# Optimization experiments

Hardware: AMD Instinct MI355X
Metric: run time of the kernel (lower is better)

The kernel has to match this reference:

```python
import jax, jax.numpy as jnp
import numpy as np

W, H = 1920, 1080
WEIGHT = 0.2          # self.weight
CONT_W = 0.1          # continuity_weight
RANK_M = 1e-4         # ranking_margin
CONT_M = 1e-4         # continuity_margin
SAMPLE_RATIO = 0.25
R = 3                 # knn_crop_radius
PAD_VAL = -1000000.0


def setup_inputs() -> dict:
    key = jax.random.key(0)
    k1, k2, k3 = jax.random.split(key, 3)
    return {
        "target_depths": jax.random.uniform(k1, (1, H * W), dtype=jnp.float32) * 100.0,
        "render_depths": jax.random.uniform(k2, (H * W,), dtype=jnp.float32) * 100.0,
        "valid_mask": jax.random.randint(k3, (1, H * W, 1), 0, 2, dtype=jnp.int32),
        "width": W,
        "height": H,
    }


def _sample_depth_loss_indices(depths, width, height, valid_mask, n_samples,
                               rank_patch_size, r, key):
    win = 2 * r + 1                      # 7
    top_n = int(0.3 * win * win + 1)     # 15
    ks = jax.random.split(key, 5)
    sy = jax.random.randint(ks[0], (n_samples, 1), 0, height - rank_patch_size)
    sx = jax.random.randint(ks[1], (n_samples, 1), 0, width - rank_patch_size)
    sy = sy + jax.random.randint(ks[2], (n_samples, 2), 0, rank_patch_size)
    sx = sx + jax.random.randint(ks[3], (n_samples, 2), 0, rank_patch_size)
    sample_idx = sy * width + sx                               # (n, 2)
    sampled_depth = depths[0][sample_idx]                      # (n, 2)

    padded = jnp.pad(depths.reshape(height, width), r, constant_values=PAD_VAL)
    dy = jnp.repeat(jnp.arange(win), win)                      # (49,) row offsets
    dx = jnp.tile(jnp.arange(win), win)                        # (49,) col offsets
    # padded coords: (y - r + dy) + r == y + dy
    py = sy[..., None] + dy                                    # (n, 2, 49)
    px = sx[..., None] + dx
    depth_crops = padded[py, px]                               # (n, 2, 49)

    sorted_crop_idx = jnp.argsort(jnp.abs(depth_crops - sampled_depth[..., None]), axis=-1)
    nbr_sample = jax.random.randint(ks[4], (n_samples, 2, 1), 1, top_n)
    rel = jnp.take_along_axis(sorted_crop_idx, nbr_sample, axis=-1)[..., 0]  # (n, 2)
    ny = sy - r + rel // win
    nx = sx - r + rel % win
    neighbours_idx = ny * width + nx                           # (n, 2)

    vm = valid_mask[0].astype(bool)                            # (H*W, C)
    samples_mask = vm[sample_idx].any(-1).all(-1)              # (n,)
    neighbours_mask = vm[neighbours_idx].any(-1).all(-1)
    full_mask = samples_mask & neighbours_mask

    # per-pair descending sort by sampled target depth
    order = jnp.argsort(-sampled_depth, axis=-1)
    s_sorted = jnp.take_along_axis(sample_idx, order, axis=-1)
    n_sorted = jnp.take_along_axis(neighbours_idx, order, axis=-1)
    idx4 = jnp.concatenate([s_sorted, n_sorted], axis=-1)      # (n, 4)
    return idx4, full_mask


def reference(target_depths, render_depths, valid_mask, width, height):
    n_samples = int(width * height * SAMPLE_RATIO)
    rank_patch_size = width // 8
    idx4, mask = _sample_depth_loss_indices(
        target_depths, width, height, valid_mask, n_samples, rank_patch_size,
        R, jax.random.key(42))
    d = render_depths[idx4].reshape(-1, 2, 2)                  # (n, 2, 2)
    rank = jnp.maximum(d[:, 0, 0] - d[:, 0, 1] + RANK_M, 0.0)  # (n,)
    cont = jnp.maximum(jnp.abs(d[:, 0, :] - d[:, 1, :]) - CONT_M, 0.0)  # (n, 2)
    # masked means == torch's boolean filtering followed by .mean()
    m = mask.astype(rank.dtype)
    denom = jnp.maximum(m.sum(), 1.0)
    rank_mean = (rank * m).sum() / denom
    cont_mean = (cont * m[:, None]).sum() / (denom * 2.0)
    return jnp.stack([WEIGHT * rank_mean, WEIGHT * CONT_W * cont_mean])
```

## Files before the change

### kernel.cpp

```cpp
#include <hip/hip_runtime.h>
#include <stdint.h>


#define IMG_W 1920
#define IMG_H 1080
#define N_PIX (IMG_W * IMG_H)
#define N_SAMP 518400
#define SEG    2025
#define PAD_VAL (-1000000.0f)
#define PW 968
#define PH 1088
#define PAD16 0xC974u

typedef uint32_t u32x4 __attribute__((ext_vector_type(4)));

struct Keys { uint32_t k[5][2][2]; };

static __host__ __device__ inline void tf2x32(uint32_t k0, uint32_t k1,
                                              uint32_t x0, uint32_t x1,
                                              uint32_t& o0, uint32_t& o1)
{
  const uint32_t ks2 = k0 ^ k1 ^ 0x1BD11BDAu;
  x0 += k0; x1 += k1;
#define TFR(r) { x0 += x1; x1 = (x1 << (r)) | (x1 >> (32 - (r))); x1 ^= x0; }
  TFR(13) TFR(15) TFR(26) TFR(6)
  x0 += k1;  x1 += ks2 + 1u;
  TFR(17) TFR(29) TFR(16) TFR(24)
  x0 += ks2; x1 += k0 + 2u;
  TFR(13) TFR(15) TFR(26) TFR(6)
  x0 += k0;  x1 += k1 + 3u;
  TFR(17) TFR(29) TFR(16) TFR(24)
  x0 += k1;  x1 += ks2 + 4u;
  TFR(13) TFR(15) TFR(26) TFR(6)
  x0 += ks2; x1 += k0 + 5u;
#undef TFR
  o0 = x0; o1 = x1;
}

__device__ __forceinline__ uint32_t jrbits(const uint32_t kk[2], uint32_t f)
{
  uint32_t a, b;
  tf2x32(kk[0], kk[1], 0u, f, a, b);
  return a ^ b;
}

__device__ __forceinline__ uint32_t jrandint(const Keys& K, int r, uint32_t f,
                                             uint32_t span)
{
  const uint32_t hi = jrbits(K.k[r][0], f);
  const uint32_t lo = jrbits(K.k[r][1], f);
  uint32_t m = 65536u % span;
  m = (m * m) % span;
  return ((hi % span) * m + (lo % span)) % span;
}

static void compute_keys(Keys& K)
{
  uint32_t ks[5][2];
  for (uint32_t t = 0; t < 5; t++) {
    uint32_t a, b; tf2x32(0u, 42u, 0u, t, a, b);
    ks[t][0] = a; ks[t][1] = b;
  }
  for (int r = 0; r < 5; r++) {
    uint32_t a, b;
    tf2x32(ks[r][0], ks[r][1], 0u, 0u, a, b); K.k[r][0][0] = a; K.k[r][0][1] = b;
    tf2x32(ks[r][0], ks[r][1], 0u, 1u, a, b); K.k[r][1][0] = a; K.k[r][1][1] = b;
  }
}

__device__ __forceinline__ bool bittest(const unsigned long long* __restrict__ vb,
                                        uint32_t idx)
{
  return ((vb[idx >> 6] >> (idx & 63u)) & 1ull) != 0ull;
}

__global__ __launch_bounds__(256) void gs_bitpack(
    const int* __restrict__ vmask,
    unsigned long long* __restrict__ vbits)
{
  const uint32_t gid = blockIdx.x * 256u + threadIdx.x;
  const unsigned long long ball = __ballot(vmask[gid] != 0);
  if ((threadIdx.x & 63u) == 0) vbits[gid >> 6] = ball;
}

__global__ __launch_bounds__(256) void gs_pack16(
    const float* __restrict__ tgt,
    uint32_t* __restrict__ t16p)
{
  const uint32_t w = blockIdx.x * 256u + threadIdx.x;
  if (w >= (uint32_t)(PW * PH)) return;
  const uint32_t wy = w / PW, wx = w % PW;
  const int sy  = (int)wy - 4;
  const int sx0 = 2 * (int)wx - 4;
  uint32_t lo = PAD16, hi = PAD16;
  if (sy >= 0 && sy < IMG_H) {
    const uint32_t* src = (const uint32_t*)tgt + (size_t)sy * IMG_W;
    if (sx0     >= 0 && sx0     < IMG_W) lo = src[sx0] >> 16;
    if (sx0 + 1 >= 0 && sx0 + 1 < IMG_W) hi = src[sx0 + 1] >> 16;
  }
  t16p[w] = lo | (hi << 16);
}

__global__ __launch_bounds__(256) void gs_sample(
    const unsigned long long* __restrict__ vbits,
    uint32_t* __restrict__ bcount,
    unsigned long long* __restrict__ wlist,
    Keys K)
{
  __shared__ unsigned long long ent[256];
  __shared__ uint32_t scnt[4];

  const uint32_t tid  = threadIdx.x;
  const uint32_t lane = tid & 63u;
  const uint32_t wave = tid >> 6;
  const uint32_t ui   = blockIdx.x * 256u + tid;

  const uint32_t syb  = jrandint(K, 0, ui, 840u);
  const uint32_t sxb  = jrandint(K, 1, ui, 1680u);
  const uint32_t oy0  = jrandint(K, 2, 2u * ui,      240u);
  const uint32_t oy1  = jrandint(K, 2, 2u * ui + 1u, 240u);
  const uint32_t ox0  = jrandint(K, 3, 2u * ui,      240u);
  const uint32_t ox1  = jrandint(K, 3, 2u * ui + 1u, 240u);
  const uint32_t nb0  = jrandint(K, 4, 2u * ui,      14u);
  const uint32_t nb1  = jrandint(K, 4, 2u * ui + 1u, 14u);
  asm volatile("" :: "v"(syb), "v"(sxb), "v"(oy0), "v"(oy1),
                     "v"(ox0), "v"(ox1), "v"(nb0), "v"(nb1));

  const uint32_t sy0 = syb + oy0, sy1 = syb + oy1;
  const uint32_t sx0 = sxb + ox0, sx1 = sxb + ox1;
  const bool ok = bittest(vbits, sy0 * IMG_W + sx0) &&
                  bittest(vbits, sy1 * IMG_W + sx1);

  const unsigned long long ball = __ballot(ok);
  if (lane == 0) scnt[wave] = (uint32_t)__popcll(ball);
  __syncthreads();

  uint32_t base = 0;
#pragma unroll
  for (uint32_t w = 0; w < 4; w++) if (w < wave) base += scnt[w];
  const uint32_t nsurv = scnt[0] + scnt[1] + scnt[2] + scnt[3];

  if (ok) {
    const uint32_t pos = base + (uint32_t)__popcll(ball & ((1ull << lane) - 1ull));
    ent[pos] = ((unsigned long long)(1u + nb1) << 48) |
               ((unsigned long long)(1u + nb0) << 44) |
               ((unsigned long long)sy0 << 33) | ((unsigned long long)sx0 << 22) |
               ((unsigned long long)sy1 << 11) |  (unsigned long long)sx1;
  }
  if (tid == 0) bcount[blockIdx.x] = nsurv;
  __syncthreads();

  unsigned long long* wb = wlist + (size_t)blockIdx.x * 256u;
  for (uint32_t t = tid; t < nsurv; t += 256u)
    wb[t] = ent[t];
}

__device__ __forceinline__ int crop_neighbor16(
    const uint32_t* __restrict__ t16p, int sy, int sx,
    float& sd_out, uint32_t nbr)
{
  const int prow0 = sy + 1;
  const int pcol  = sx + 1;
  const int ex    = pcol & ~1;
  const uint32_t s = (uint32_t)(pcol & 1);
  const uint32_t* p = t16p + (size_t)prow0 * PW + (ex >> 1);

  u32x4 R0, R1, R2, R3, R4, R5, R6;
  asm volatile(
      "global_load_dwordx4 %0, %7, off\n\t"
      "global_load_dwordx4 %1, %8, off\n\t"
      "global_load_dwordx4 %2, %9, off\n\t"
      "global_load_dwordx4 %3, %10, off\n\t"
      "global_load_dwordx4 %4, %11, off\n\t"
      "global_load_dwordx4 %5, %12, off\n\t"
      "global_load_dwordx4 %6, %13, off\n\t"
      "s_waitcnt vmcnt(0)"
      : "=&v"(R0), "=&v"(R1), "=&v"(R2), "=&v"(R3),
        "=&v"(R4), "=&v"(R5), "=&v"(R6)
      : "v"(p), "v"(p + PW), "v"(p + 2 * PW), "v"(p + 3 * PW),
        "v"(p + 4 * PW), "v"(p + 5 * PW), "v"(p + 6 * PW));

  const uint32_t sdbits = s ? (R3[2] << 16) : (R3[1] & 0xFFFF0000u);
  const float sd = __uint_as_float(sdbits);
  sd_out = sd;

  const u32x4 R[7] = { R0, R1, R2, R3, R4, R5, R6 };

  uint32_t arr[15];
#pragma unroll
  for (int t = 0; t < 15; t++) arr[t] = 0xFFFFFFFFu;

#pragma unroll
  for (int r = 0; r < 7; r++) {
    const u32x4 W = R[r];
#pragma unroll
    for (int c = 0; c < 7; c++) {
      uint32_t bits;
      if (c & 1) bits = s ? (W[(c + 1) >> 1] << 16) : (W[c >> 1] & 0xFFFF0000u);
      else       bits = s ? (W[c >> 1] & 0xFFFF0000u) : (W[c >> 1] << 16);
      const float v = __uint_as_float(bits);
      const int q = r * 7 + c;
      uint32_t key = (__float_as_uint(v - sd) & 0x7FFFFFC0u) | (uint32_t)q;
      const int depth = (q + 1 < 15) ? (q + 1) : 15;
#pragma unroll
      for (int t = 0; t < 15; t++) {
        if (t < depth) {
          const uint32_t lo = min(key, arr[t]);
          const uint32_t hi = max(key, arr[t]);
          arr[t] = lo; key = hi;
        }
      }
    }
  }

  uint32_t relkey = 0;
#pragma unroll
  for (int t = 1; t < 15; t++)
    if ((uint32_t)t == nbr) relkey = arr[t];
  const uint32_t rel = relkey & 63u;
  return (sy - 3 + (int)(rel / 7u)) * IMG_W + (sx - 3 + (int)(rel % 7u));
}

__global__ __launch_bounds__(256, 4) void gs_crop(
    const uint32_t* __restrict__ t16p,
    const float* __restrict__ rnd,
    const unsigned long long* __restrict__ vbits,
    const uint32_t* __restrict__ bcount,
    const unsigned long long* __restrict__ wlist,
    float* __restrict__ acc)
{
  __shared__ float partial[12];
  const uint32_t tid  = threadIdx.x;
  const uint32_t lane = tid & 63u;
  const uint32_t wave = tid >> 6;

  const uint32_t seg0 = 2u * blockIdx.x;
  const uint32_t c0 = bcount[seg0];
  const uint32_t c1 = (seg0 + 1 < SEG) ? bcount[seg0 + 1] : 0;
  const uint32_t m  = 2u * (c0 + c1);

  float rank_a = 0.f, cont_a = 0.f, cnt_a = 0.f;
  for (uint32_t t = tid; t < ((m + 255u) & ~255u); t += 256u) {
    float sd = 0.f, r = 0.f, q = 0.f;
    bool v = false;
    if (t < m) {
      const uint32_t tc0 = 2u * c0;
      const unsigned long long e = (t < tc0)
          ? wlist[(size_t)seg0 * 256u + (t >> 1)]
          : wlist[(size_t)(seg0 + 1) * 256u + ((t - tc0) >> 1)];
      const int j = (int)(t & 1u);
      const int sy  = j ? (int)((e >> 11) & 2047u) : (int)((e >> 33) & 2047u);
      const int sx  = j ? (int)( e        & 2047u) : (int)((e >> 22) & 2047u);
      const uint32_t nbr = j ? (uint32_t)((e >> 48) & 15u)
                             : (uint32_t)((e >> 44) & 15u);
      r = rnd[sy * IMG_W + sx];
      const int nidx = crop_neighbor16(t16p, sy, sx, sd, nbr);
      v = bittest(vbits, (uint32_t)nidx);
      q = rnd[nidx];
    }

    const float psd = __shfl_xor(sd, 1);
    const float pr  = __shfl_xor(r, 1);
    const bool  pv  = (bool)__shfl_xor((int)v, 1);
    const bool pairok = (t < m) && v && pv;

    cont_a += pairok ? fmaxf(fabsf(r - q) - 1e-4f, 0.f) : 0.f;
    if (pairok && ((t & 1u) == 0)) {
      const bool keep = sd >= psd;
      const float ra = keep ? r : pr;
      const float rb = keep ? pr : r;
      rank_a += fmaxf(ra - rb + 1e-4f, 0.f);
      cnt_a  += 1.f;
    }
  }

#pragma unroll
  for (int off = 32; off > 0; off >>= 1) {
    rank_a += __shfl_down(rank_a, off);
    cont_a += __shfl_down(cont_a, off);
    cnt_a  += __shfl_down(cnt_a, off);
  }
  if (lane == 0) {
    partial[wave * 3 + 0] = rank_a;
    partial[wave * 3 + 1] = cont_a;
    partial[wave * 3 + 2] = cnt_a;
  }
  __syncthreads();
  if (tid < 3) {
    const float sm = partial[tid] + partial[3 + tid] +
                     partial[6 + tid] + partial[9 + tid];
    atomicAdd(acc + tid, sm);
  }
}

__device__ __forceinline__ int crop_neighbor32(const float* __restrict__ tgt,
                                               int sy, int sx, float sd,
                                               uint32_t nbr)
{
  float v[7][8];
  const bool interior = (sy >= 3) && (sy <= IMG_H - 4) &&
                        (sx >= 3) && (sx <= IMG_W - 5);
  if (interior) {
    const float* p = tgt + (sy - 3) * IMG_W + (sx - 3);
#pragma unroll
    for (int r = 0; r < 7; r++)
      __builtin_memcpy(&v[r][0], p + r * IMG_W, 32);
  } else {
#pragma unroll
    for (int r = 0; r < 7; r++) {
      const int yy = sy - 3 + r;
      const bool rok = (yy >= 0) && (yy < IMG_H);
#pragma unroll
      for (int c = 0; c < 8; c++) {
        const int xx = sx - 3 + c;
        const bool okc = rok && (c < 7) && (xx >= 0) && (xx < IMG_W);
        v[r][c] = okc ? tgt[yy * IMG_W + xx] : PAD_VAL;
      }
    }
  }
  uint32_t arr[15];
#pragma unroll
  for (int t = 0; t < 15; t++) arr[t] = 0xFFFFFFFFu;
#pragma unroll
  for (int r = 0; r < 7; r++) {
#pragma unroll
    for (int c = 0; c < 7; c++) {
      const int q = r * 7 + c;
      uint32_t key = (__float_as_uint(v[r][c] - sd) & 0x7FFFFFC0u) | (uint32_t)q;
      const int depth = (q + 1 < 15) ? (q + 1) : 15;
#pragma unroll
      for (int t = 0; t < 15; t++) {
        if (t < depth) {
          const uint32_t lo = min(key, arr[t]);
          const uint32_t hi = max(key, arr[t]);
          arr[t] = lo; key = hi;
        }
      }
    }
  }
  uint32_t relkey = 0;
#pragma unroll
  for (int t = 1; t < 15; t++)
    if ((uint32_t)t == nbr) relkey = arr[t];
  const uint32_t rel = relkey & 63u;
  return (sy - 3 + (int)(rel / 7u)) * IMG_W + (sx - 3 + (int)(rel % 7u));
}

__global__ __launch_bounds__(256, 2) void gs_fused(
    const float* __restrict__ tgt,
    const float* __restrict__ rnd,
    const int*   __restrict__ vmask,
    float* __restrict__ acc,
    Keys K)
{
  __shared__ float partial[12];
  const uint32_t tid  = threadIdx.x;
  const uint32_t lane = tid & 63u;
  const uint32_t wave = tid >> 6;
  const uint32_t ui   = blockIdx.x * 256u + tid;

  float rank_c = 0.f, cont_c = 0.f, cnt_c = 0.f;
  if (ui < N_SAMP) {
    const uint32_t syb = jrandint(K, 0, ui, 840u);
    const uint32_t sxb = jrandint(K, 1, ui, 1680u);
    int sy[2], sx[2], sidx[2];
    float sd[2];
    bool sm = true;
#pragma unroll
    for (int j = 0; j < 2; j++) {
      sy[j] = (int)(syb + jrandint(K, 2, 2u * ui + (uint32_t)j, 240u));
      sx[j] = (int)(sxb + jrandint(K, 3, 2u * ui + (uint32_t)j, 240u));
      sidx[j] = sy[j] * IMG_W + sx[j];
      sd[j] = tgt[sidx[j]];
      sm = sm && (vmask[sidx[j]] != 0);
    }
    if (sm) {
      int nidx[2]; bool nm = true;
#pragma unroll
      for (int j = 0; j < 2; j++) {
        const uint32_t nbr = 1u + jrandint(K, 4, 2u * ui + (uint32_t)j, 14u);
        nidx[j] = crop_neighbor32(tgt, sy[j], sx[j], sd[j], nbr);
        nm = nm && (vmask[nidx[j]] != 0);
      }
      if (nm) {
        const float r0 = rnd[sidx[0]], r1 = rnd[sidx[1]];
        const float q0 = rnd[nidx[0]], q1 = rnd[nidx[1]];
        const bool keep = sd[0] >= sd[1];
        const float ra = keep ? r0 : r1;
        const float rb = keep ? r1 : r0;
        rank_c = fmaxf(ra - rb + 1e-4f, 0.f);
        cont_c = fmaxf(fabsf(r0 - q0) - 1e-4f, 0.f)
               + fmaxf(fabsf(r1 - q1) - 1e-4f, 0.f);
        cnt_c = 1.f;
      }
    }
  }
#pragma unroll
  for (int off = 32; off > 0; off >>= 1) {
    rank_c += __shfl_down(rank_c, off);
    cont_c += __shfl_down(cont_c, off);
    cnt_c  += __shfl_down(cnt_c, off);
  }
  if (lane == 0) {
    partial[wave * 3 + 0] = rank_c;
    partial[wave * 3 + 1] = cont_c;
    partial[wave * 3 + 2] = cnt_c;
  }
  __syncthreads();
  if (tid < 3) {
    const float sm2 = partial[tid] + partial[3 + tid] +
                      partial[6 + tid] + partial[9 + tid];
    atomicAdd(acc + tid, sm2);
  }
}

__global__ void gs_finalize(const float* __restrict__ acc, float* __restrict__ out)
{
  const float denom = fmaxf(acc[2], 1.0f);
  out[0] = 0.2f * (acc[0] / denom);
  out[1] = 0.2f * 0.1f * (acc[1] / (denom * 2.0f));
}

extern "C" void kernel_launch(void* const* d_in, const int* in_sizes, int n_in,
                              void* d_out, int out_size, void* d_ws, size_t ws_size,
                              hipStream_t stream)
{
  (void)in_sizes; (void)n_in; (void)out_size;
  const float* tgt   = (const float*)d_in[0];
  const float* rnd   = (const float*)d_in[1];
  const int*   vmask = (const int*)d_in[2];
  float* out = (float*)d_out;

  char* p = (char*)d_ws;
  float*    acc   = (float*)p;
  unsigned long long* vbits = (unsigned long long*)(p + 16);
  uint32_t* t16p  = (uint32_t*)(p + 16 + 259200);
  uint32_t* bcount = (uint32_t*)(p + 16 + 259200 + 4213504);
  unsigned long long* wlist =
      (unsigned long long*)(p + 16 + 259200 + 4213504 + 8112);
  const size_t need = 16 + 259200 + 4213504 + 8112 + (size_t)SEG * 256 * 8;

  Keys K;
  compute_keys(K);

  hipMemsetAsync(acc, 0, 16, stream);

  if (ws_size >= need) {
    gs_bitpack<<<N_PIX / 256, 256, 0, stream>>>(vmask, vbits);
    gs_pack16<<<(PW * PH + 255) / 256, 256, 0, stream>>>(tgt, t16p);
    gs_sample<<<SEG, 256, 0, stream>>>(vbits, bcount, wlist, K);
    gs_crop<<<(SEG + 1) / 2, 256, 0, stream>>>(t16p, rnd, vbits, bcount,
                                               wlist, acc);
  } else {
    gs_fused<<<N_SAMP / 256, 256, 0, stream>>>(tgt, rnd, vmask, acc, K);
  }
  gs_finalize<<<1, 1, 0, stream>>>(acc, out);
}
```

Before: 68.57 us.

## Fuse sampling, crop and finalize into one kernel; merge prep kernels

Merges bitpack and pack16 into a single prep kernel that also zeroes the accumulator header, replacing the memset. The sampling and crop stages now run in one kernel that compacts surviving pairs in shared memory, and the last block to finish writes the final outputs, so the global worklist round-trip and three launches go away. The per-neighbour random draw is recomputed after compaction rather than stored, and launch bounds drop to 2 blocks per SM. The cost is more shared memory, lower occupancy and a serialised last-block finalize.

New measurement: 85.64 us. 1.25x slower.

```diff
diff --git a/kernel.cpp b/kernel.cpp
--- a/kernel.cpp
+++ b/kernel.cpp
@@ -6,13 +6,14 @@
 #define IMG_H 1080
 #define N_PIX (IMG_W * IMG_H)
 #define N_SAMP 518400
-#define SEG    2025
+#define MAIN_BLKS 1013
 #define PAD_VAL (-1000000.0f)
 #define PW 968
 #define PH 1088
 #define PAD16 0xC974u
 
 typedef uint32_t u32x4 __attribute__((ext_vector_type(4)));
+typedef unsigned long long ull;
 
 struct Keys { uint32_t k[5][2][2]; };
 
@@ -68,91 +69,35 @@
   }
 }
 
-__device__ __forceinline__ bool bittest(const unsigned long long* __restrict__ vb,
-                                        uint32_t idx)
+__device__ __forceinline__ bool bittest(const ull* __restrict__ vb, uint32_t idx)
 {
   return ((vb[idx >> 6] >> (idx & 63u)) & 1ull) != 0ull;
 }
 
-__global__ __launch_bounds__(256) void gs_bitpack(
-    const int* __restrict__ vmask,
-    unsigned long long* __restrict__ vbits)
+__global__ __launch_bounds__(256) void gs_prep(
+    const int*   __restrict__ vmask,
+    const float* __restrict__ tgt,
+    ull*      __restrict__ vbits,
+    uint32_t* __restrict__ t16p,
+    uint32_t* __restrict__ hdr)
 {
   const uint32_t gid = blockIdx.x * 256u + threadIdx.x;
-  const unsigned long long ball = __ballot(vmask[gid] != 0);
+  const ull ball = __ballot(vmask[gid] != 0);
   if ((threadIdx.x & 63u) == 0) vbits[gid >> 6] = ball;
-}
-
-__global__ __launch_bounds__(256) void gs_pack16(
-    const float* __restrict__ tgt,
-    uint32_t* __restrict__ t16p)
-{
-  const uint32_t w = blockIdx.x * 256u + threadIdx.x;
-  if (w >= (uint32_t)(PW * PH)) return;
-  const uint32_t wy = w / PW, wx = w % PW;
-  const int sy  = (int)wy - 4;
-  const int sx0 = 2 * (int)wx - 4;
-  uint32_t lo = PAD16, hi = PAD16;
-  if (sy >= 0 && sy < IMG_H) {
-    const uint32_t* src = (const uint32_t*)tgt + (size_t)sy * IMG_W;
-    if (sx0     >= 0 && sx0     < IMG_W) lo = src[sx0] >> 16;
-    if (sx0 + 1 >= 0 && sx0 + 1 < IMG_W) hi = src[sx0 + 1] >> 16;
-  }
-  t16p[w] = lo | (hi << 16);
-}
-
-__global__ __launch_bounds__(256) void gs_sample(
-    const unsigned long long* __restrict__ vbits,
-    uint32_t* __restrict__ bcount,
-    unsigned long long* __restrict__ wlist,
-    Keys K)
-{
-  __shared__ unsigned long long ent[256];
-  __shared__ uint32_t scnt[4];
-
-  const uint32_t tid  = threadIdx.x;
-  const uint32_t lane = tid & 63u;
-  const uint32_t wave = tid >> 6;
-  const uint32_t ui   = blockIdx.x * 256u + tid;
-
-  const uint32_t syb  = jrandint(K, 0, ui, 840u);
-  const uint32_t sxb  = jrandint(K, 1, ui, 1680u);
-  const uint32_t oy0  = jrandint(K, 2, 2u * ui,      240u);
-  const uint32_t oy1  = jrandint(K, 2, 2u * ui + 1u, 240u);
-  const uint32_t ox0  = jrandint(K, 3, 2u * ui,      240u);
-  const uint32_t ox1  = jrandint(K, 3, 2u * ui + 1u, 240u);
-  const uint32_t nb0  = jrandint(K, 4, 2u * ui,      14u);
-  const uint32_t nb1  = jrandint(K, 4, 2u * ui + 1u, 14u);
-  asm volatile("" :: "v"(syb), "v"(sxb), "v"(oy0), "v"(oy1),
-                     "v"(ox0), "v"(ox1), "v"(nb0), "v"(nb1));
-
-  const uint32_t sy0 = syb + oy0, sy1 = syb + oy1;
-  const uint32_t sx0 = sxb + ox0, sx1 = sxb + ox1;
-  const bool ok = bittest(vbits, sy0 * IMG_W + sx0) &&
-                  bittest(vbits, sy1 * IMG_W + sx1);
-
-  const unsigned long long ball = __ballot(ok);
-  if (lane == 0) scnt[wave] = (uint32_t)__popcll(ball);
-  __syncthreads();
-
-  uint32_t base = 0;
-#pragma unroll
-  for (uint32_t w = 0; w < 4; w++) if (w < wave) base += scnt[w];
-  const uint32_t nsurv = scnt[0] + scnt[1] + scnt[2] + scnt[3];
-
-  if (ok) {
-    const uint32_t pos = base + (uint32_t)__popcll(ball & ((1ull << lane) - 1ull));
-    ent[pos] = ((unsigned long long)(1u + nb1) << 48) |
-               ((unsigned long long)(1u + nb0) << 44) |
-               ((unsigned long long)sy0 << 33) | ((unsigned long long)sx0 << 22) |
-               ((unsigned long long)sy1 << 11) |  (unsigned long long)sx1;
-  }
-  if (tid == 0) bcount[blockIdx.x] = nsurv;
-  __syncthreads();
-
-  unsigned long long* wb = wlist + (size_t)blockIdx.x * 256u;
-  for (uint32_t t = tid; t < nsurv; t += 256u)
-    wb[t] = ent[t];
+
+  if (gid < (uint32_t)(PW * PH)) {
+    const uint32_t wy = gid / PW, wx = gid % PW;
+    const int sy  = (int)wy - 4;
+    const int sx0 = 2 * (int)wx - 4;
+    uint32_t lo = PAD16, hi = PAD16;
+    if (sy >= 0 && sy < IMG_H) {
+      const uint32_t* src = (const uint32_t*)tgt + (size_t)sy * IMG_W;
+      if (sx0     >= 0 && sx0     < IMG_W) lo = src[sx0] >> 16;
+      if (sx0 + 1 >= 0 && sx0 + 1 < IMG_W) hi = src[sx0 + 1] >> 16;
+    }
+    t16p[gid] = lo | (hi << 16);
+  }
+  if (gid < 4) hdr[gid] = 0;
 }
 
 __device__ __forceinline__ int crop_neighbor16(
@@ -221,75 +166,138 @@
   return (sy - 3 + (int)(rel / 7u)) * IMG_W + (sx - 3 + (int)(rel % 7u));
 }
 
-__global__ __launch_bounds__(256, 4) void gs_crop(
+__global__ __launch_bounds__(256, 2) void gs_main(
     const uint32_t* __restrict__ t16p,
     const float* __restrict__ rnd,
-    const unsigned long long* __restrict__ vbits,
-    const uint32_t* __restrict__ bcount,
-    const unsigned long long* __restrict__ wlist,
-    float* __restrict__ acc)
-{
-  __shared__ float partial[12];
+    const ull*   __restrict__ vbits,
+    float* __restrict__ acc,
+    float* __restrict__ out,
+    Keys K)
+{
+  __shared__ ull      ent[512];
+  __shared__ float    res_sd[1024];
+  __shared__ int      res_ni[1024];
+  __shared__ uint32_t scnt[8];
+  __shared__ float    partial[12];
+
   const uint32_t tid  = threadIdx.x;
   const uint32_t lane = tid & 63u;
   const uint32_t wave = tid >> 6;
 
-  const uint32_t seg0 = 2u * blockIdx.x;
-  const uint32_t c0 = bcount[seg0];
-  const uint32_t c1 = (seg0 + 1 < SEG) ? bcount[seg0 + 1] : 0;
-  const uint32_t m  = 2u * (c0 + c1);
-
-  float rank_a = 0.f, cont_a = 0.f, cnt_a = 0.f;
-  for (uint32_t t = tid; t < ((m + 255u) & ~255u); t += 256u) {
-    float sd = 0.f, r = 0.f, q = 0.f;
-    bool v = false;
-    if (t < m) {
-      const uint32_t tc0 = 2u * c0;
-      const unsigned long long e = (t < tc0)
-          ? wlist[(size_t)seg0 * 256u + (t >> 1)]
-          : wlist[(size_t)(seg0 + 1) * 256u + ((t - tc0) >> 1)];
-      const int j = (int)(t & 1u);
-      const int sy  = j ? (int)((e >> 11) & 2047u) : (int)((e >> 33) & 2047u);
-      const int sx  = j ? (int)( e        & 2047u) : (int)((e >> 22) & 2047u);
-      const uint32_t nbr = j ? (uint32_t)((e >> 48) & 15u)
-                             : (uint32_t)((e >> 44) & 15u);
-      r = rnd[sy * IMG_W + sx];
-      const int nidx = crop_neighbor16(t16p, sy, sx, sd, nbr);
-      v = bittest(vbits, (uint32_t)nidx);
-      q = rnd[nidx];
-    }
-
-    const float psd = __shfl_xor(sd, 1);
-    const float pr  = __shfl_xor(r, 1);
-    const bool  pv  = (bool)__shfl_xor((int)v, 1);
-    const bool pairok = (t < m) && v && pv;
-
-    cont_a += pairok ? fmaxf(fabsf(r - q) - 1e-4f, 0.f) : 0.f;
-    if (pairok && ((t & 1u) == 0)) {
-      const bool keep = sd >= psd;
-      const float ra = keep ? r : pr;
-      const float rb = keep ? pr : r;
-      rank_a += fmaxf(ra - rb + 1e-4f, 0.f);
-      cnt_a  += 1.f;
+  ull eb[2];
+  bool ok[2];
+#pragma unroll
+  for (int h = 0; h < 2; h++) {
+    const uint32_t ui = blockIdx.x * 512u + (uint32_t)h * 256u + tid;
+    bool o = false;
+    ull ee = 0;
+    if (ui < N_SAMP) {
+      const uint32_t syb = jrandint(K, 0, ui, 840u);
+      const uint32_t sxb = jrandint(K, 1, ui, 1680u);
+      const uint32_t oy0 = jrandint(K, 2, 2u * ui,      240u);
+      const uint32_t oy1 = jrandint(K, 2, 2u * ui + 1u, 240u);
+      const uint32_t ox0 = jrandint(K, 3, 2u * ui,      240u);
+      const uint32_t ox1 = jrandint(K, 3, 2u * ui + 1u, 240u);
+      asm volatile("" :: "v"(syb), "v"(sxb), "v"(oy0), "v"(oy1),
+                         "v"(ox0), "v"(ox1));
+      const uint32_t sy0 = syb + oy0, sy1 = syb + oy1;
+      const uint32_t sx0 = sxb + ox0, sx1 = sxb + ox1;
+      o = bittest(vbits, sy0 * IMG_W + sx0) &&
+          bittest(vbits, sy1 * IMG_W + sx1);
+      ee = ((ull)ui << 44) |
+           ((ull)sy0 << 33) | ((ull)sx0 << 22) |
+           ((ull)sy1 << 11) |  (ull)sx1;
+    }
+    ok[h] = o; eb[h] = ee;
+  }
+
+  const ull b0 = __ballot(ok[0]);
+  const ull b1 = __ballot(ok[1]);
+  if (lane == 0) {
+    scnt[wave]     = (uint32_t)__popcll(b0);
+    scnt[4 + wave] = (uint32_t)__popcll(b1);
+  }
+  __syncthreads();
+
+  uint32_t base0 = 0, sum0 = 0, base1 = 0, nsurv = 0;
+#pragma unroll
+  for (uint32_t w = 0; w < 4; w++) {
+    if (w < wave) { base0 += scnt[w]; base1 += scnt[4 + w]; }
+    sum0  += scnt[w];
+    nsurv += scnt[w] + scnt[4 + w];
+  }
+  base1 += sum0;
+
+  if (ok[0]) ent[base0 + (uint32_t)__popcll(b0 & ((1ull << lane) - 1ull))] = eb[0];
+  if (ok[1]) ent[base1 + (uint32_t)__popcll(b1 & ((1ull << lane) - 1ull))] = eb[1];
+  __syncthreads();
+
+  for (uint32_t t = tid; t < 2u * nsurv; t += 256u) {
+    const ull ee = ent[t >> 1];
+    const int jj = (int)(t & 1u);
+    const uint32_t eui = (uint32_t)(ee >> 44);
+    const int sy = jj ? (int)((ee >> 11) & 2047u) : (int)((ee >> 33) & 2047u);
+    const int sx = jj ? (int)( ee        & 2047u) : (int)((ee >> 22) & 2047u);
+    const uint32_t nbr = 1u + jrandint(K, 4, 2u * eui + (uint32_t)jj, 14u);
+    float sd;
+    const int nidx = crop_neighbor16(t16p, sy, sx, sd, nbr);
+    res_sd[t] = sd;
+    res_ni[t] = bittest(vbits, (uint32_t)nidx) ? nidx : -1;
+  }
+  __syncthreads();
+
+  float rank_c = 0.f, cont_c = 0.f, cnt_c = 0.f;
+  for (uint32_t sI = tid; sI < nsurv; sI += 256u) {
+    const int n0 = res_ni[2u * sI], n1 = res_ni[2u * sI + 1u];
+    if ((n0 >= 0) && (n1 >= 0)) {
+      const ull ee = ent[sI];
+      const int esy0 = (int)((ee >> 33) & 2047u), esx0 = (int)((ee >> 22) & 2047u);
+      const int esy1 = (int)((ee >> 11) & 2047u), esx1 = (int)( ee        & 2047u);
+      const float r0 = rnd[esy0 * IMG_W + esx0];
+      const float r1 = rnd[esy1 * IMG_W + esx1];
+      const float q0 = rnd[n0], q1 = rnd[n1];
+      const float sd0 = res_sd[2u * sI], sd1 = res_sd[2u * sI + 1u];
+      const bool keep = sd0 >= sd1;
+      const float ra = keep ? r0 : r1;
+      const float rb = keep ? r1 : r0;
+      rank_c += fmaxf(ra - rb + 1e-4f, 0.f);
+      cont_c += fmaxf(fabsf(r0 - q0) - 1e-4f, 0.f)
+              + fmaxf(fabsf(r1 - q1) - 1e-4f, 0.f);
+      cnt_c  += 1.f;
     }
   }
 
 #pragma unroll
   for (int off = 32; off > 0; off >>= 1) {
-    rank_a += __shfl_down(rank_a, off);
-    cont_a += __shfl_down(cont_a, off);
-    cnt_a  += __shfl_down(cnt_a, off);
+    rank_c += __shfl_down(rank_c, off);
+    cont_c += __shfl_down(cont_c, off);
+    cnt_c  += __shfl_down(cnt_c, off);
   }
   if (lane == 0) {
-    partial[wave * 3 + 0] = rank_a;
-    partial[wave * 3 + 1] = cont_a;
-    partial[wave * 3 + 2] = cnt_a;
+    partial[wave * 3 + 0] = rank_c;
+    partial[wave * 3 + 1] = cont_c;
+    partial[wave * 3 + 2] = cnt_c;
   }
   __syncthreads();
-  if (tid < 3) {
-    const float sm = partial[tid] + partial[3 + tid] +
-                     partial[6 + tid] + partial[9 + tid];
-    atomicAdd(acc + tid, sm);
+  if (tid == 0) {
+    const float s0 = partial[0] + partial[3] + partial[6] + partial[9];
+    const float s1 = partial[1] + partial[4] + partial[7] + partial[10];
+    const float s2 = partial[2] + partial[5] + partial[8] + partial[11];
+    atomicAdd(acc + 0, s0);
+    atomicAdd(acc + 1, s1);
+    atomicAdd(acc + 2, s2);
+    __threadfence();
+    uint32_t* done = (uint32_t*)acc + 3;
+    const uint32_t old = atomicAdd(done, 1u);
+    if (old == (uint32_t)gridDim.x - 1u) {
+      __threadfence();
+      const float a0 = atomicAdd(acc + 0, 0.f);
+      const float a1 = atomicAdd(acc + 1, 0.f);
+      const float a2 = atomicAdd(acc + 2, 0.f);
+      const float denom = fmaxf(a2, 1.0f);
+      out[0] = 0.2f  * (a0 / denom);
+      out[1] = 0.02f * (a1 / (denom * 2.0f));
+    }
   }
 }
 
@@ -417,8 +425,8 @@
 __global__ void gs_finalize(const float* __restrict__ acc, float* __restrict__ out)
 {
   const float denom = fmaxf(acc[2], 1.0f);
-  out[0] = 0.2f * (acc[0] / denom);
-  out[1] = 0.2f * 0.1f * (acc[1] / (denom * 2.0f));
+  out[0] = 0.2f  * (acc[0] / denom);
+  out[1] = 0.02f * (acc[1] / (denom * 2.0f));
 }
 
 extern "C" void kernel_launch(void* const* d_in, const int* in_sizes, int n_in,
@@ -433,26 +441,20 @@
 
   char* p = (char*)d_ws;
   float*    acc   = (float*)p;
-  unsigned long long* vbits = (unsigned long long*)(p + 16);
+  ull*      vbits = (ull*)(p + 16);
   uint32_t* t16p  = (uint32_t*)(p + 16 + 259200);
-  uint32_t* bcount = (uint32_t*)(p + 16 + 259200 + 4213504);
-  unsigned long long* wlist =
-      (unsigned long long*)(p + 16 + 259200 + 4213504 + 8112);
-  const size_t need = 16 + 259200 + 4213504 + 8112 + (size_t)SEG * 256 * 8;
+  const size_t need = 16 + 259200 + 4213504;
 
   Keys K;
   compute_keys(K);
 
-  hipMemsetAsync(acc, 0, 16, stream);
-
   if (ws_size >= need) {
-    gs_bitpack<<<N_PIX / 256, 256, 0, stream>>>(vmask, vbits);
-    gs_pack16<<<(PW * PH + 255) / 256, 256, 0, stream>>>(tgt, t16p);
-    gs_sample<<<SEG, 256, 0, stream>>>(vbits, bcount, wlist, K);
-    gs_crop<<<(SEG + 1) / 2, 256, 0, stream>>>(t16p, rnd, vbits, bcount,
-                                               wlist, acc);
+    gs_prep<<<N_PIX / 256, 256, 0, stream>>>(vmask, tgt, vbits, t16p,
+                                             (uint32_t*)acc);
+    gs_main<<<MAIN_BLKS, 256, 0, stream>>>(t16p, rnd, vbits, acc, out, K);
   } else {
+    hipMemsetAsync(acc, 0, 16, stream);
     gs_fused<<<N_SAMP / 256, 256, 0, stream>>>(tgt, rnd, vmask, acc, K);
-  }
-  gs_finalize<<<1, 1, 0, stream>>>(acc, out);
-}
+    gs_finalize<<<1, 1, 0, stream>>>(acc, out);
+  }
+}
```
